# Performance work log

Measured on AMD Instinct MI355X. Metric: run time of the kernel, lower is better.

## Reference

```python
import jax, jax.numpy as jnp
import numpy as np

B = 4
N_TOTAL = 40000
N_SRC0, N_DST0, E0 = 30000, 15000, 360000
N_DST1, E1 = 7500, 180000
D_IN, OUT = 64, 32
H1, C1 = 8, 8
H2, C2 = 1, OUT
NEG_SLOPE = 0.2


def setup_inputs() -> dict:
    key = jax.random.key(0)
    ks = jax.random.split(key, 16)
    inp = {
        'x': jax.random.normal(ks[0], (B, N_TOTAL, D_IN), dtype=jnp.float32),
        'n_id0': jax.random.randint(ks[1], (N_SRC0,), 0, N_SRC0),
        'res_n_id0': jax.random.randint(ks[2], (N_DST0,), 0, N_SRC0),
        'edge_src0': jax.random.randint(ks[3], (E0,), 0, N_SRC0),
        'edge_dst0': jax.random.randint(ks[4], (E0,), 0, N_DST0),
        'res_n_id1': jax.random.randint(ks[5], (N_DST1,), 0, N_DST0),
        'edge_src1': jax.random.randint(ks[6], (E1,), 0, N_DST0),
        'edge_dst1': jax.random.randint(ks[7], (E1,), 0, N_DST1),
        # GATConv params (Glorot-ish scale)
        'W1': jax.random.normal(ks[8], (D_IN, H1 * C1), dtype=jnp.float32) / np.sqrt(D_IN),
        'att_src1': jax.random.normal(ks[9], (H1, C1), dtype=jnp.float32) / np.sqrt(C1),
        'att_dst1': jax.random.normal(ks[10], (H1, C1), dtype=jnp.float32) / np.sqrt(C1),
        'b1': jnp.zeros((H1 * C1,), dtype=jnp.float32),
        'W2': jax.random.normal(ks[11], (H1 * C1, H2 * C2), dtype=jnp.float32) / np.sqrt(H1 * C1),
        'att_src2': jax.random.normal(ks[12], (H2, C2), dtype=jnp.float32) / np.sqrt(C2),
        'att_dst2': jax.random.normal(ks[13], (H2, C2), dtype=jnp.float32) / np.sqrt(C2),
        'b2': jnp.zeros((H2 * C2,), dtype=jnp.float32),
    }
    return inp


def gat_conv(x_src, x_dst, src, dst, W, a_src, a_dst, bias, n_dst, H, C):
    """Bipartite PyG-style GATConv (concat=True, eval mode, no self-loops)."""
    b = x_src.shape[0]
    hs = (x_src @ W).reshape(b, -1, H, C)            # [B, Ns, H, C]
    hd = (x_dst @ W).reshape(b, -1, H, C)            # [B, Nd, H, C]
    es = jnp.einsum('bnhc,hc->bnh', hs, a_src)       # [B, Ns, H]
    ed = jnp.einsum('bnhc,hc->bnh', hd, a_dst)       # [B, Nd, H]
    e = jax.nn.leaky_relu(es[:, src] + ed[:, dst], NEG_SLOPE)  # [B, E, H]
    eT = jnp.swapaxes(e, 0, 1)                       # [E, B, H] (segment over axis 0)
    m = jax.ops.segment_max(eT, dst, num_segments=n_dst)
    p = jnp.exp(eT - m[dst])
    den = jax.ops.segment_sum(p, dst, num_segments=n_dst)
    alpha = p / den[dst]                             # [E, B, H]
    msg = alpha[..., None] * jnp.swapaxes(hs[:, src], 0, 1)    # [E, B, H, C]
    out = jax.ops.segment_sum(msg, dst, num_segments=n_dst)    # [Nd, B, H, C]
    out = jnp.swapaxes(out, 0, 1).reshape(b, n_dst, H * C)
    return out + bias


def reference(x, n_id0, res_n_id0, edge_src0, edge_dst0, res_n_id1, edge_src1,
              edge_dst1, W1, att_src1, att_dst1, b1, W2, att_src2, att_dst2, b2):
    xt = x[:, n_id0, :]                                        # [B, N_SRC0, D_IN]
    h = gat_conv(xt, xt[:, res_n_id0, :], edge_src0, edge_dst0,
                 W1, att_src1, att_dst1, b1, N_DST0, H1, C1)
    h = jax.nn.elu(h)                                          # dropout = identity (eval)
    out = gat_conv(h, h[:, res_n_id1, :], edge_src1, edge_dst1,
                   W2, att_src2, att_dst2, b2, N_DST1, H2, C2)
    return out                                                 # [B, N_DST1, OUT]
```

## Files before the change

kernel.cpp:

```cpp
#include <hip/hip_runtime.h>

#define NB 4
#define NT 40000
#define NS0 30000
#define ND0 15000
#define NE0 360000
#define ND1 7500
#define NE1 180000
#define NEG 0.2f

#define CAP 64
#define K1B ((NB*NS0)/64)
#define SB8 ((NE0 + NE1 + 2047)/2048)
#define K3PB 938
#define K7PB 469

typedef __attribute__((ext_vector_type(8))) short bf8;
typedef __attribute__((ext_vector_type(4))) float f4;
typedef __attribute__((ext_vector_type(2))) float f2;

__device__ __forceinline__ unsigned short f2bf(float f) {
    unsigned u = __float_as_uint(f);
    u += 0x7FFF + ((u >> 16) & 1);
    return (unsigned short)(u >> 16);
}
__device__ __forceinline__ f2 upk(unsigned u) {
    f2 r;
    r.x = __uint_as_float(u << 16);
    r.y = __uint_as_float(u & 0xFFFF0000u);
    return r;
}

__global__ __launch_bounds__(256) void kA_gemm_scat(
        const float* __restrict__ x, const int* __restrict__ n_id0,
        const float* __restrict__ W1, const float* __restrict__ a_src,
        const float* __restrict__ a_dst,
        unsigned short* __restrict__ ht1b, float* __restrict__ es1, float* __restrict__ ed1,
        const int* __restrict__ esrc0, const int* __restrict__ edst0,
        const int* __restrict__ esrc1, const int* __restrict__ edst1,
        int* __restrict__ cur0, int* __restrict__ cur1,
        int* __restrict__ srcsort0, int* __restrict__ srcsort1) {
    __shared__ unsigned short xtb[64*72];
    __shared__ unsigned short wtb[64*72];
    __shared__ float asl[64], adl[64];
    if (blockIdx.x >= K1B) {
        int base = (blockIdx.x - K1B) * 2048 + threadIdx.x;
        #pragma unroll
        for (int p = 0; p < 8; ++p) {
            int t = base + p * 256;
            if (t < NE0) {
                int d = edst0[t];
                int pos = atomicAdd(&cur0[d], 1);
                if (pos < CAP) srcsort0[d*CAP + pos] = esrc0[t];
            } else if (t < NE0 + NE1) {
                int e = t - NE0;
                int d = edst1[e];
                int pos = atomicAdd(&cur1[d], 1);
                if (pos < CAP) srcsort1[d*CAP + pos] = esrc1[e];
            }
        }
        return;
    }
    int bid = blockIdx.x;
    int t = threadIdx.x;
    {
        int k = t >> 2, nb = (t & 3) * 16;
        const float* wrow = &W1[k*64 + nb];
        #pragma unroll
        for (int j = 0; j < 16; j += 4) {
            float4 v = *(const float4*)&wrow[j];
            wtb[(nb+j+0)*72 + k] = f2bf(v.x);
            wtb[(nb+j+1)*72 + k] = f2bf(v.y);
            wtb[(nb+j+2)*72 + k] = f2bf(v.z);
            wtb[(nb+j+3)*72 + k] = f2bf(v.w);
        }
    }
    if (t < 64) { asl[t] = a_src[t]; adl[t] = a_dst[t]; }
    {
        int r   = t >> 2;
        int sub = t & 3;
        int row_s = bid * 64 + r;
        int bs = row_s / NS0;
        int ns = row_s - bs * NS0;
        const float* xrow = x + ((size_t)(bs * NT + n_id0[ns])) * 64;
        #pragma unroll
        for (int j = 0; j < 4; ++j) {
            int kf = (sub + j*4) * 4;
            float4 v = *(const float4*)&xrow[kf];
            ushort4 u;
            u.x = f2bf(v.x); u.y = f2bf(v.y); u.z = f2bf(v.z); u.w = f2bf(v.w);
            *(ushort4*)&xtb[r*72 + kf] = u;
        }
    }
    __syncthreads();
    int w = t >> 6, lane = t & 63, quad = lane >> 4, cl = lane & 15;
    int arow = 16*w + cl;
    bf8 a0 = *(const bf8*)&xtb[arow*72 + quad*8];
    bf8 a1 = *(const bf8*)&xtb[arow*72 + 32 + quad*8];
    f4 acc[4];
    #pragma unroll
    for (int sub = 0; sub < 4; ++sub) {
        int n = sub*16 + cl;
        bf8 b0 = *(const bf8*)&wtb[n*72 + quad*8];
        bf8 b1v = *(const bf8*)&wtb[n*72 + 32 + quad*8];
        f4 c = {0.f, 0.f, 0.f, 0.f};
        c = __builtin_amdgcn_mfma_f32_16x16x32_bf16(a0, b0, c, 0, 0, 0);
        c = __builtin_amdgcn_mfma_f32_16x16x32_bf16(a1, b1v, c, 0, 0, 0);
        acc[sub] = c;
    }
    __syncthreads();
    unsigned short* ob = xtb;
    #pragma unroll
    for (int sub = 0; sub < 4; ++sub)
        #pragma unroll
        for (int r = 0; r < 4; ++r)
            ob[(16*w + 4*quad + r)*64 + sub*16 + cl] = f2bf(acc[sub][r]);
    int rbase = bid*64 + 16*w + quad*4;
    #pragma unroll
    for (int r = 0; r < 4; ++r) {
        #pragma unroll
        for (int sub = 0; sub < 4; ++sub) {
            int col = sub*16 + cl;
            float ps = acc[sub][r] * asl[col];
            float pd = acc[sub][r] * adl[col];
            ps += __shfl_xor(ps, 1); ps += __shfl_xor(ps, 2); ps += __shfl_xor(ps, 4);
            pd += __shfl_xor(pd, 1); pd += __shfl_xor(pd, 2); pd += __shfl_xor(pd, 4);
            if ((cl & 7) == 0) {
                int h = sub*2 + (cl >> 3);
                es1[(rbase + r)*8 + h] = ps;
                ed1[(rbase + r)*8 + h] = pd;
            }
        }
    }
    __syncthreads();
    {
        int row = t >> 3;
        int c8  = t & 7;
        #pragma unroll
        for (int rep = 0; rep < 2; ++rep) {
            int rr2 = row + rep*32;
            uint4 v = *(const uint4*)&ob[rr2*64 + c8*8];
            *(uint4*)&ht1b[((size_t)(bid*64 + rr2))*64 + c8*8] = v;
        }
    }
}

__global__ __launch_bounds__(1024) void k3_agg1_node2(
        const int* __restrict__ srcsort0, const int* __restrict__ cur0,
        const int* __restrict__ res0,
        const float* __restrict__ es1, const float* __restrict__ ed1,
        const unsigned short* __restrict__ ht1b, const float* __restrict__ b1,
        const float* __restrict__ W2, const float* __restrict__ a_src2,
        const float* __restrict__ a_dst2,
        float* __restrict__ ht2, float* __restrict__ es2, float* __restrict__ ed2) {
    __shared__ float W2t[32][68];
    __shared__ float as2[32], ad2[32];
    __shared__ float b1l[64];
    __shared__ float hsh[16][64];
    int t = threadIdx.x;
    if (t < 256) {
        float4 v0 = *(const float4*)&W2[t*8];
        float4 v1 = *(const float4*)&W2[t*8 + 4];
        int k = t >> 2, c = (t & 3) * 8;
        W2t[c+0][k] = v0.x; W2t[c+1][k] = v0.y; W2t[c+2][k] = v0.z; W2t[c+3][k] = v0.w;
        W2t[c+4][k] = v1.x; W2t[c+5][k] = v1.y; W2t[c+6][k] = v1.z; W2t[c+7][k] = v1.w;
    }
    if (t < 32) { as2[t] = a_src2[t]; ad2[t] = a_dst2[t]; }
    if (t < 64) b1l[t] = b1[t];
    __syncthreads();
    int b = blockIdx.x / K3PB;
    int local = blockIdx.x - b * K3PB;
    int wv = t >> 6;
    int d = local * 16 + wv;
    if (d >= ND0) return;
    int lane = t & 63;
    int grp = lane >> 3;
    int c = lane & 7;
    int dn = res0[d];
    float edv = ed1[(b*NS0 + dn)*8 + c];
    int start = d * CAP;
    int cnt = cur0[d];
    const float* esb = es1 + (size_t)b*NS0*8;
    const unsigned short* htb = ht1b + (size_t)b*NS0*64;
    f2 a01 = {0.f, 0.f}, a23 = {0.f, 0.f}, a45 = {0.f, 0.f}, a67 = {0.f, 0.f};
    float wsum = 0.f;
    int i = grp;
    bool v0 = i      < cnt, v1 = i + 8  < cnt,
         v2 = i + 16 < cnt, v3 = i + 24 < cnt;
    int s0 = v0 ? srcsort0[start + i]      : 0;
    int s1 = v1 ? srcsort0[start + i + 8]  : 0;
    int s2 = v2 ? srcsort0[start + i + 16] : 0;
    int s3 = v3 ? srcsort0[start + i + 24] : 0;
    for (;;) {
        float e0 = esb[s0*8 + c], e1 = esb[s1*8 + c];
        float e2 = esb[s2*8 + c], e3 = esb[s3*8 + c];
        uint4 h0 = *(const uint4*)&htb[(size_t)s0*64 + c*8];
        uint4 h1 = *(const uint4*)&htb[(size_t)s1*64 + c*8];
        uint4 h2 = *(const uint4*)&htb[(size_t)s2*64 + c*8];
        uint4 h3 = *(const uint4*)&htb[(size_t)s3*64 + c*8];
        int ni = i + 32;
        bool nv0 = false, nv1 = false, nv2 = false, nv3 = false;
        int t0 = 0, t1 = 0, t2 = 0, t3 = 0;
        if (ni < cnt) {
            nv0 = true;            nv1 = ni + 8  < cnt;
            nv2 = ni + 16 < cnt;   nv3 = ni + 24 < cnt;
            t0 =       srcsort0[start + ni];
            t1 = nv1 ? srcsort0[start + ni + 8]  : 0;
            t2 = nv2 ? srcsort0[start + ni + 16] : 0;
            t3 = nv3 ? srcsort0[start + ni + 24] : 0;
        }
        e0 += edv; e1 += edv; e2 += edv; e3 += edv;
        e0 = e0 > 0.f ? e0 : NEG * e0;
        e1 = e1 > 0.f ? e1 : NEG * e1;
        e2 = e2 > 0.f ? e2 : NEG * e2;
        e3 = e3 > 0.f ? e3 : NEG * e3;
        float w0 = v0 ? __expf(e0) : 0.f;
        float w1 = v1 ? __expf(e1) : 0.f;
        float w2 = v2 ? __expf(e2) : 0.f;
        float w3 = v3 ? __expf(e3) : 0.f;
        a01 += w0 * upk(h0.x); a23 += w0 * upk(h0.y);
        a45 += w0 * upk(h0.z); a67 += w0 * upk(h0.w);
        a01 += w1 * upk(h1.x); a23 += w1 * upk(h1.y);
        a45 += w1 * upk(h1.z); a67 += w1 * upk(h1.w);
        a01 += w2 * upk(h2.x); a23 += w2 * upk(h2.y);
        a45 += w2 * upk(h2.z); a67 += w2 * upk(h2.w);
        a01 += w3 * upk(h3.x); a23 += w3 * upk(h3.y);
        a45 += w3 * upk(h3.z); a67 += w3 * upk(h3.w);
        wsum += (w0 + w1) + (w2 + w3);
        i = ni; s0 = t0; s1 = t1; s2 = t2; s3 = t3;
        v0 = nv0; v1 = nv1; v2 = nv2; v3 = nv3;
        if (i >= cnt) break;
    }
    float acc[8] = {a01.x, a01.y, a23.x, a23.y, a45.x, a45.y, a67.x, a67.y};
    int g0 = grp & 1, g1 = (grp >> 1) & 1, g2 = grp >> 2;
    float n0, n1, n2, n3;
    {
        float s, r;
        s = g0 ? acc[0] : acc[1]; r = __shfl_xor(s, 8);  n0 = (g0 ? acc[1] : acc[0]) + r;
        s = g0 ? acc[2] : acc[3]; r = __shfl_xor(s, 8);  n1 = (g0 ? acc[3] : acc[2]) + r;
        s = g0 ? acc[4] : acc[5]; r = __shfl_xor(s, 8);  n2 = (g0 ? acc[5] : acc[4]) + r;
        s = g0 ? acc[6] : acc[7]; r = __shfl_xor(s, 8);  n3 = (g0 ? acc[7] : acc[6]) + r;
    }
    float m0, m1;
    {
        float s, r;
        s = g1 ? n0 : n1; r = __shfl_xor(s, 16); m0 = (g1 ? n1 : n0) + r;
        s = g1 ? n2 : n3; r = __shfl_xor(s, 16); m1 = (g1 ? n3 : n2) + r;
    }
    float fin;
    {
        float s = g2 ? m0 : m1; float r = __shfl_xor(s, 32); fin = (g2 ? m1 : m0) + r;
    }
    wsum += __shfl_xor(wsum, 8); wsum += __shfl_xor(wsum, 16); wsum += __shfl_xor(wsum, 32);
    float inv = cnt > 0 ? 1.f / wsum : 0.f;
    float o = fin * inv + b1l[(c << 3) | grp];
    o = o > 0.f ? o : __expf(o) - 1.f;
    hsh[wv][(c << 3) | grp] = o;
    int c2 = lane & 31, half = lane >> 5;
    const float4* hp = (const float4*)&hsh[wv][half * 32];
    const float4* wp = (const float4*)&W2t[c2][half * 32];
    float acc2 = 0.f;
    #pragma unroll
    for (int q = 0; q < 8; ++q) {
        float4 hv = hp[q];
        float4 w4 = wp[q];
        acc2 = fmaf(hv.x, w4.x, acc2); acc2 = fmaf(hv.y, w4.y, acc2);
        acc2 = fmaf(hv.z, w4.z, acc2); acc2 = fmaf(hv.w, w4.w, acc2);
    }
    acc2 += __shfl_xor(acc2, 32);
    float ps = acc2 * as2[c2];
    float pd = acc2 * ad2[c2];
    ps += __shfl_xor(ps, 1); ps += __shfl_xor(ps, 2); ps += __shfl_xor(ps, 4);
    ps += __shfl_xor(ps, 8); ps += __shfl_xor(ps, 16);
    pd += __shfl_xor(pd, 1); pd += __shfl_xor(pd, 2); pd += __shfl_xor(pd, 4);
    pd += __shfl_xor(pd, 8); pd += __shfl_xor(pd, 16);
    int row = b*ND0 + d;
    if (half == 0) ht2[(size_t)row*32 + c2] = acc2;
    if (lane == 0) { es2[row] = ps; ed2[row] = pd; }
}

__global__ __launch_bounds__(1024) void k7_agg2(
        const int* __restrict__ srcsort1, const int* __restrict__ cur1,
        const int* __restrict__ res1,
        const float* __restrict__ es2, const float* __restrict__ ed2,
        const float* __restrict__ ht2, const float* __restrict__ b2,
        float* __restrict__ outp) {
    int b = blockIdx.x / K7PB;
    int local = blockIdx.x - b * K7PB;
    int wv = threadIdx.x >> 6;
    int d = local * 16 + wv;
    if (d >= ND1) return;
    int lane = threadIdx.x & 63;
    int grp = lane >> 3;
    int c = lane & 7;
    int dn = res1[d];
    float edv = ed2[b*ND0 + dn];
    int start = d * CAP;
    int cnt = cur1[d];
    const float* esb = es2 + (size_t)b*ND0;
    const float* htb = ht2 + (size_t)b*ND0*32;
    f4 accv = {0.f, 0.f, 0.f, 0.f};
    float wsum = 0.f;
    int i = grp;
    bool v0 = i      < cnt, v1 = i + 8  < cnt,
         v2 = i + 16 < cnt, v3 = i + 24 < cnt;
    int s0 = v0 ? srcsort1[start + i]      : 0;
    int s1 = v1 ? srcsort1[start + i + 8]  : 0;
    int s2 = v2 ? srcsort1[start + i + 16] : 0;
    int s3 = v3 ? srcsort1[start + i + 24] : 0;
    for (;;) {
        float lg0 = esb[s0], lg1 = esb[s1], lg2 = esb[s2], lg3 = esb[s3];
        f4 h0 = *(const f4*)&htb[(size_t)s0*32 + c*4];
        f4 h1 = *(const f4*)&htb[(size_t)s1*32 + c*4];
        f4 h2 = *(const f4*)&htb[(size_t)s2*32 + c*4];
        f4 h3 = *(const f4*)&htb[(size_t)s3*32 + c*4];
        int ni = i + 32;
        bool nv0 = false, nv1 = false, nv2 = false, nv3 = false;
        int t0 = 0, t1 = 0, t2 = 0, t3 = 0;
        if (ni < cnt) {
            nv0 = true;            nv1 = ni + 8  < cnt;
            nv2 = ni + 16 < cnt;   nv3 = ni + 24 < cnt;
            t0 =       srcsort1[start + ni];
            t1 = nv1 ? srcsort1[start + ni + 8]  : 0;
            t2 = nv2 ? srcsort1[start + ni + 16] : 0;
            t3 = nv3 ? srcsort1[start + ni + 24] : 0;
        }
        lg0 += edv; lg1 += edv; lg2 += edv; lg3 += edv;
        lg0 = lg0 > 0.f ? lg0 : NEG * lg0;
        lg1 = lg1 > 0.f ? lg1 : NEG * lg1;
        lg2 = lg2 > 0.f ? lg2 : NEG * lg2;
        lg3 = lg3 > 0.f ? lg3 : NEG * lg3;
        float w0 = v0 ? __expf(lg0) : 0.f;
        float w1 = v1 ? __expf(lg1) : 0.f;
        float w2 = v2 ? __expf(lg2) : 0.f;
        float w3 = v3 ? __expf(lg3) : 0.f;
        accv += w0 * h0;
        accv += w1 * h1;
        accv += w2 * h2;
        accv += w3 * h3;
        wsum += (w0 + w1) + (w2 + w3);
        i = ni; s0 = t0; s1 = t1; s2 = t2; s3 = t3;
        v0 = nv0; v1 = nv1; v2 = nv2; v3 = nv3;
        if (i >= cnt) break;
    }
    float ax = accv.x, ay = accv.y, az = accv.z, aw = accv.w;
    ax += __shfl_xor(ax, 8); ax += __shfl_xor(ax, 16); ax += __shfl_xor(ax, 32);
    ay += __shfl_xor(ay, 8); ay += __shfl_xor(ay, 16); ay += __shfl_xor(ay, 32);
    az += __shfl_xor(az, 8); az += __shfl_xor(az, 16); az += __shfl_xor(az, 32);
    aw += __shfl_xor(aw, 8); aw += __shfl_xor(aw, 16); aw += __shfl_xor(aw, 32);
    wsum += __shfl_xor(wsum, 8); wsum += __shfl_xor(wsum, 16); wsum += __shfl_xor(wsum, 32);
    if (grp == 0) {
        float inv = cnt > 0 ? 1.f / wsum : 0.f;
        float4 bb = *(const float4*)&b2[c*4];
        float4 o;
        o.x = ax*inv + bb.x; o.y = ay*inv + bb.y;
        o.z = az*inv + bb.z; o.w = aw*inv + bb.w;
        *(float4*)&outp[((size_t)(b*ND1 + d))*32 + c*4] = o;
    }
}

extern "C" void kernel_launch(void* const* d_in, const int* in_sizes, int n_in,
                              void* d_out, int out_size, void* d_ws, size_t ws_size,
                              hipStream_t stream) {
    const float* x        = (const float*)d_in[0];
    const int*   n_id0    = (const int*)d_in[1];
    const int*   res0     = (const int*)d_in[2];
    const int*   esrc0    = (const int*)d_in[3];
    const int*   edst0    = (const int*)d_in[4];
    const int*   res1     = (const int*)d_in[5];
    const int*   esrc1    = (const int*)d_in[6];
    const int*   edst1    = (const int*)d_in[7];
    const float* W1       = (const float*)d_in[8];
    const float* a_src1   = (const float*)d_in[9];
    const float* a_dst1   = (const float*)d_in[10];
    const float* b1       = (const float*)d_in[11];
    const float* W2       = (const float*)d_in[12];
    const float* a_src2   = (const float*)d_in[13];
    const float* a_dst2   = (const float*)d_in[14];
    const float* b2       = (const float*)d_in[15];
    float* outp = (float*)d_out;

    char* base = (char*)d_ws;
    unsigned short* ht1b = (unsigned short*)base;
    float* es1  = (float*)(base + 15360000);
    float* ed1  = es1 + 960000;
    float* ht2  = ed1 + 960000;
    float* es2  = ht2 + 1920000;
    float* ed2  = es2 + 60000;
    int* cur0     = (int*)(ed2 + 60000);
    int* cur1     = cur0 + ND0;
    int* srcsort0 = cur1 + ND1;
    int* srcsort1 = srcsort0 + ND0*CAP;

    hipMemsetAsync(cur0, 0, (ND0 + ND1) * sizeof(int), stream);
    kA_gemm_scat<<<K1B + SB8, 256, 0, stream>>>(x, n_id0, W1, a_src1, a_dst1,
                                                ht1b, es1, ed1,
                                                esrc0, edst0, esrc1, edst1,
                                                cur0, cur1, srcsort0, srcsort1);
    k3_agg1_node2<<<NB*K3PB, 1024, 0, stream>>>(srcsort0, cur0, res0, es1, ed1, ht1b, b1,
                                                W2, a_src2, a_dst2, ht2, es2, ed2);
    k7_agg2<<<NB*K7PB, 1024, 0, stream>>>(srcsort1, cur1, res1, es2, ed2, ht2, b2, outp);
}
```

Measured before the change: 198.4 us.

## Bucket-transpose edge lists for vector index loads and XCD-aware block mapping

Edge slots are stored in a transposed order (pos%8 major), so each lane group can fetch its four source indices with a single int4 load instead of four scalar loads. The aggregation kernels shrink from 1024-thread to 256-thread blocks, and a block-to-(batch, chunk) mapping keyed on blockIdx&7 keeps each batch's gathered data on a pair of XCDs to improve L2 locality. Counts are clamped to CAP, and the kernels still rely on ND0 and ND1 dividing evenly into 4-node chunks.

```diff
diff --git a/kernel.cpp b/kernel.cpp
--- a/kernel.cpp
+++ b/kernel.cpp
@@ -12,8 +12,8 @@
 #define CAP 64
 #define K1B ((NB*NS0)/64)
 #define SB8 ((NE0 + NE1 + 2047)/2048)
-#define K3PB 938
-#define K7PB 469
+
+#define BKT(p) ((((p) & 7) << 3) | ((p) >> 3))
 
 typedef __attribute__((ext_vector_type(8))) short bf8;
 typedef __attribute__((ext_vector_type(4))) float f4;
@@ -51,12 +51,12 @@
             if (t < NE0) {
                 int d = edst0[t];
                 int pos = atomicAdd(&cur0[d], 1);
-                if (pos < CAP) srcsort0[d*CAP + pos] = esrc0[t];
+                if (pos < CAP) srcsort0[d*CAP + BKT(pos)] = esrc0[t];
             } else if (t < NE0 + NE1) {
                 int e = t - NE0;
                 int d = edst1[e];
                 int pos = atomicAdd(&cur1[d], 1);
-                if (pos < CAP) srcsort1[d*CAP + pos] = esrc1[e];
+                if (pos < CAP) srcsort1[d*CAP + BKT(pos)] = esrc1[e];
             }
         }
         return;
@@ -145,7 +145,7 @@
     }
 }
 
-__global__ __launch_bounds__(1024) void k3_agg1_node2(
+__global__ __launch_bounds__(256) void k3_agg1_node2(
         const int* __restrict__ srcsort0, const int* __restrict__ cur0,
         const int* __restrict__ res0,
         const float* __restrict__ es1, const float* __restrict__ ed1,
@@ -156,9 +156,9 @@
     __shared__ float W2t[32][68];
     __shared__ float as2[32], ad2[32];
     __shared__ float b1l[64];
-    __shared__ float hsh[16][64];
+    __shared__ float hsh[4][64];
     int t = threadIdx.x;
-    if (t < 256) {
+    {
         float4 v0 = *(const float4*)&W2[t*8];
         float4 v1 = *(const float4*)&W2[t*8 + 4];
         int k = t >> 2, c = (t & 3) * 8;
@@ -168,29 +168,31 @@
     if (t < 32) { as2[t] = a_src2[t]; ad2[t] = a_dst2[t]; }
     if (t < 64) b1l[t] = b1[t];
     __syncthreads();
-    int b = blockIdx.x / K3PB;
-    int local = blockIdx.x - b * K3PB;
+    int xcd = blockIdx.x & 7;
+    int b = xcd >> 1;
+    int chunk = (blockIdx.x >> 3) * 2 + (xcd & 1);
     int wv = t >> 6;
-    int d = local * 16 + wv;
-    if (d >= ND0) return;
+    int d = chunk * 4 + wv;
     int lane = t & 63;
     int grp = lane >> 3;
     int c = lane & 7;
     int dn = res0[d];
     float edv = ed1[(b*NS0 + dn)*8 + c];
     int start = d * CAP;
-    int cnt = cur0[d];
+    int cnt = min(cur0[d], CAP);
     const float* esb = es1 + (size_t)b*NS0*8;
     const unsigned short* htb = ht1b + (size_t)b*NS0*64;
     f2 a01 = {0.f, 0.f}, a23 = {0.f, 0.f}, a45 = {0.f, 0.f}, a67 = {0.f, 0.f};
     float wsum = 0.f;
     int i = grp;
+    int pp = start + grp*8;
+    int4 sv = *(const int4*)&srcsort0[pp];
     bool v0 = i      < cnt, v1 = i + 8  < cnt,
          v2 = i + 16 < cnt, v3 = i + 24 < cnt;
-    int s0 = v0 ? srcsort0[start + i]      : 0;
-    int s1 = v1 ? srcsort0[start + i + 8]  : 0;
-    int s2 = v2 ? srcsort0[start + i + 16] : 0;
-    int s3 = v3 ? srcsort0[start + i + 24] : 0;
+    int s0 = v0 ? sv.x : 0;
+    int s1 = v1 ? sv.y : 0;
+    int s2 = v2 ? sv.z : 0;
+    int s3 = v3 ? sv.w : 0;
     for (;;) {
         float e0 = esb[s0*8 + c], e1 = esb[s1*8 + c];
         float e2 = esb[s2*8 + c], e3 = esb[s3*8 + c];
@@ -202,12 +204,13 @@
         bool nv0 = false, nv1 = false, nv2 = false, nv3 = false;
         int t0 = 0, t1 = 0, t2 = 0, t3 = 0;
         if (ni < cnt) {
+            int4 nsv = *(const int4*)&srcsort0[pp + 4];
             nv0 = true;            nv1 = ni + 8  < cnt;
             nv2 = ni + 16 < cnt;   nv3 = ni + 24 < cnt;
-            t0 =       srcsort0[start + ni];
-            t1 = nv1 ? srcsort0[start + ni + 8]  : 0;
-            t2 = nv2 ? srcsort0[start + ni + 16] : 0;
-            t3 = nv3 ? srcsort0[start + ni + 24] : 0;
+            t0 =       nsv.x;
+            t1 = nv1 ? nsv.y : 0;
+            t2 = nv2 ? nsv.z : 0;
+            t3 = nv3 ? nsv.w : 0;
         }
         e0 += edv; e1 += edv; e2 += edv; e3 += edv;
         e0 = e0 > 0.f ? e0 : NEG * e0;
@@ -227,7 +230,8 @@
         a01 += w3 * upk(h3.x); a23 += w3 * upk(h3.y);
         a45 += w3 * upk(h3.z); a67 += w3 * upk(h3.w);
         wsum += (w0 + w1) + (w2 + w3);
-        i = ni; s0 = t0; s1 = t1; s2 = t2; s3 = t3;
+        i = ni; pp += 4;
+        s0 = t0; s1 = t1; s2 = t2; s3 = t3;
         v0 = nv0; v1 = nv1; v2 = nv2; v3 = nv3;
         if (i >= cnt) break;
     }
@@ -279,35 +283,37 @@
     if (lane == 0) { es2[row] = ps; ed2[row] = pd; }
 }
 
-__global__ __launch_bounds__(1024) void k7_agg2(
+__global__ __launch_bounds__(256) void k7_agg2(
         const int* __restrict__ srcsort1, const int* __restrict__ cur1,
         const int* __restrict__ res1,
         const float* __restrict__ es2, const float* __restrict__ ed2,
         const float* __restrict__ ht2, const float* __restrict__ b2,
         float* __restrict__ outp) {
-    int b = blockIdx.x / K7PB;
-    int local = blockIdx.x - b * K7PB;
-    int wv = threadIdx.x >> 6;
-    int d = local * 16 + wv;
-    if (d >= ND1) return;
+    int xcd = blockIdx.x & 7;
+    int b = xcd >> 1;
+    int chunk = (blockIdx.x >> 3) * 2 + (xcd & 1);
+    if (chunk >= ND1/4) return;
+    int d = chunk * 4 + (threadIdx.x >> 6);
     int lane = threadIdx.x & 63;
     int grp = lane >> 3;
     int c = lane & 7;
     int dn = res1[d];
     float edv = ed2[b*ND0 + dn];
     int start = d * CAP;
-    int cnt = cur1[d];
+    int cnt = min(cur1[d], CAP);
     const float* esb = es2 + (size_t)b*ND0;
     const float* htb = ht2 + (size_t)b*ND0*32;
     f4 accv = {0.f, 0.f, 0.f, 0.f};
     float wsum = 0.f;
     int i = grp;
+    int pp = start + grp*8;
+    int4 sv = *(const int4*)&srcsort1[pp];
     bool v0 = i      < cnt, v1 = i + 8  < cnt,
          v2 = i + 16 < cnt, v3 = i + 24 < cnt;
-    int s0 = v0 ? srcsort1[start + i]      : 0;
-    int s1 = v1 ? srcsort1[start + i + 8]  : 0;
-    int s2 = v2 ? srcsort1[start + i + 16] : 0;
-    int s3 = v3 ? srcsort1[start + i + 24] : 0;
+    int s0 = v0 ? sv.x : 0;
+    int s1 = v1 ? sv.y : 0;
+    int s2 = v2 ? sv.z : 0;
+    int s3 = v3 ? sv.w : 0;
     for (;;) {
         float lg0 = esb[s0], lg1 = esb[s1], lg2 = esb[s2], lg3 = esb[s3];
         f4 h0 = *(const f4*)&htb[(size_t)s0*32 + c*4];
@@ -318,12 +324,13 @@
         bool nv0 = false, nv1 = false, nv2 = false, nv3 = false;
         int t0 = 0, t1 = 0, t2 = 0, t3 = 0;
         if (ni < cnt) {
+            int4 nsv = *(const int4*)&srcsort1[pp + 4];
             nv0 = true;            nv1 = ni + 8  < cnt;
             nv2 = ni + 16 < cnt;   nv3 = ni + 24 < cnt;
-            t0 =       srcsort1[start + ni];
-            t1 = nv1 ? srcsort1[start + ni + 8]  : 0;
-            t2 = nv2 ? srcsort1[start + ni + 16] : 0;
-            t3 = nv3 ? srcsort1[start + ni + 24] : 0;
+            t0 =       nsv.x;
+            t1 = nv1 ? nsv.y : 0;
+            t2 = nv2 ? nsv.z : 0;
+            t3 = nv3 ? nsv.w : 0;
         }
         lg0 += edv; lg1 += edv; lg2 += edv; lg3 += edv;
         lg0 = lg0 > 0.f ? lg0 : NEG * lg0;
@@ -339,7 +346,8 @@
         accv += w2 * h2;
         accv += w3 * h3;
         wsum += (w0 + w1) + (w2 + w3);
-        i = ni; s0 = t0; s1 = t1; s2 = t2; s3 = t3;
+        i = ni; pp += 4;
+        s0 = t0; s1 = t1; s2 = t2; s3 = t3;
         v0 = nv0; v1 = nv1; v2 = nv2; v3 = nv3;
         if (i >= cnt) break;
     }
@@ -397,7 +405,7 @@
                                                 ht1b, es1, ed1,
                                                 esrc0, edst0, esrc1, edst1,
                                                 cur0, cur1, srcsort0, srcsort1);
-    k3_agg1_node2<<<NB*K3PB, 1024, 0, stream>>>(srcsort0, cur0, res0, es1, ed1, ht1b, b1,
-                                                W2, a_src2, a_dst2, ht2, es2, ed2);
-    k7_agg2<<<NB*K7PB, 1024, 0, stream>>>(srcsort1, cur1, res1, es2, ed2, ht2, b2, outp);
-}
+    k3_agg1_node2<<<NB*(ND0/4), 256, 0, stream>>>(srcsort0, cur0, res0, es1, ed1, ht1b, b1,
+                                                  W2, a_src2, a_dst2, ht2, es2, ed2);
+    k7_agg2<<<7504, 256, 0, stream>>>(srcsort1, cur1, res1, es2, ed2, ht2, b2, outp);
+}
```

After: 184.1 us. 7.2% less time.
